# Kernel optimization log

Hardware: AMD Instinct MI355X
Metric: run time of the kernel (lower is better)

## Reference

```python
import jax, jax.numpy as jnp
import numpy as np
import math

N_HEAD = 16
N_EMBD = 1024
BLOCK_SIZE = 2048
B, T = 2, 2048
R = 32.0
MAX_SPAN = float(BLOCK_SIZE)
SPAN_REG = 2e-06
PERIOD_MIN, PERIOD_MAX = 2.0, 4.0
RATIO_MIN, RATIO_MAX = -0.25, 0.25


def setup_inputs() -> dict:
    key = jax.random.key(0)
    ks = jax.random.split(key, 5)
    x = jax.random.normal(ks[0], (B, T, N_EMBD), dtype=jnp.float32)
    # scale weights like nn.Linear init to keep logits sane
    w_attn = jax.random.normal(ks[1], (N_EMBD, 3 * N_EMBD), dtype=jnp.float32) * 0.02
    b_attn = jnp.zeros((3 * N_EMBD,), dtype=jnp.float32)
    w_proj = jax.random.normal(ks[2], (N_EMBD, N_EMBD), dtype=jnp.float32) * 0.02
    b_proj = jnp.zeros((N_EMBD,), dtype=jnp.float32)
    span_params = jnp.zeros((N_HEAD,), dtype=jnp.float32)
    # torch init: period uniform in [2,4] -> logit weight space; ratio 0 -> logit(0.5)=0
    init_period = jax.random.uniform(ks[3], (N_HEAD,), dtype=jnp.float32) * (PERIOD_MAX - PERIOD_MIN) + PERIOD_MIN
    pn = (init_period - PERIOD_MIN) / (PERIOD_MAX - PERIOD_MIN)
    period_weight = jnp.log(pn) - jnp.log1p(-pn)  # logit
    ratio_weight = jnp.zeros((N_HEAD,), dtype=jnp.float32)
    return {"x": x, "w_attn": w_attn, "b_attn": b_attn, "w_proj": w_proj,
            "b_proj": b_proj, "span_params": span_params,
            "period_weight": period_weight, "ratio_weight": ratio_weight}


def _forward(x, w_attn, b_attn, w_proj, b_proj, span_params, period_weight, ratio_weight):
    Bb, Tt, C = x.shape
    D = C // N_HEAD
    qkv = x @ w_attn + b_attn  # [B,T,3C]
    q, k, v = jnp.split(qkv, 3, axis=-1)
    q = q.reshape(Bb, Tt, N_HEAD, D)
    k = k.reshape(Bb, Tt, N_HEAD, D)
    v = v.reshape(Bb, Tt, N_HEAD, D)
    scale = 1.0 / math.sqrt(D)
    att = jnp.einsum('bihd,bjhd->bhij', q, k) * scale  # [B,H,T,T]

    pos = jnp.arange(Tt, dtype=jnp.float32)
    rel = pos[:, None] - pos[None, :]          # [T,T]
    causal = rel >= 0.0
    rel_c = jnp.maximum(rel, 0.0)              # clamp(min=0)

    clamped_spans = jax.nn.sigmoid(span_params) * MAX_SPAN  # [H]
    # span mask: clamp((R - rel + span)/R, 0, 1); non-causal (rel->inf) -> 0
    mask_pos = jnp.where(causal[None, :, :],
                         jnp.clip((R - rel[None, :, :] + clamped_spans[:, None, None]) / R, 0.0, 1.0),
                         0.0)  # [H,T,T]

    period = PERIOD_MIN + (PERIOD_MAX - PERIOD_MIN) * jax.nn.sigmoid(period_weight)  # [H]
    ratio = RATIO_MIN + (RATIO_MAX - RATIO_MIN) * jax.nn.sigmoid(ratio_weight)       # [H]
    amplitude = period / 4.0
    offset = period * ratio
    wave = 0.5 * (jnp.cos(2.0 * math.pi * rel_c[None, :, :] / period[:, None, None]) + 1.0) \
           * amplitude[:, None, None] + 0.5 + offset[:, None, None]
    wave = jnp.clip(wave, 0.0, 1.0)  # [H,T,T]
    loss_terms = 1.0 / period + 2.0 * ratio - 1.0 / PERIOD_MAX - 2.0 * RATIO_MIN  # [H]

    mask = mask_pos * wave  # [H,T,T]

    att = jnp.where(causal[None, None, :, :], att, -jnp.inf)
    att_max = jnp.max(att, axis=-1, keepdims=True)
    att_exp = jnp.exp(att - att_max)
    weighted = att_exp * mask[None]  # [B,H,T,T]
    att = weighted / jnp.sum(weighted, axis=-1, keepdims=True)

    y = jnp.einsum('bhij,bjhd->bihd', att, v).reshape(Bb, Tt, C)
    y = y @ w_proj + b_proj

    span_loss = SPAN_REG * jnp.sum((clamped_spans + R) * loss_terms) / N_HEAD
    return y, span_loss


def reference(x, w_attn, b_attn, w_proj, b_proj, span_params, period_weight, ratio_weight):
    return _forward(x, w_attn, b_attn, w_proj, b_proj, span_params, period_weight, ratio_weight)
```

## Files before the change

kernel.cpp:

```cpp
#include <hip/hip_runtime.h>
#include <math.h>
#include <float.h>

#define NHEAD 16
#define DHEAD 64
#define SEQT  2048
#define NB    2
#define CEMB  1024
#define C3    3072

typedef __attribute__((ext_vector_type(8))) short  s16x8;
typedef __attribute__((ext_vector_type(4))) short  s16x4;
typedef __attribute__((ext_vector_type(8))) unsigned short u16x8;
typedef __attribute__((ext_vector_type(4))) unsigned short u16x4;
typedef __attribute__((ext_vector_type(4))) float  f32x4;

__device__ __forceinline__ float sigmoidf_(float x) { return 1.0f / (1.0f + expf(-x)); }

__device__ __forceinline__ unsigned short f2b(float f) {
    __bf16 b = (__bf16)f;
    return __builtin_bit_cast(unsigned short, b);
}

__device__ __forceinline__ void gload16(const void* g, void* l) {
    __builtin_amdgcn_global_load_lds(
        (const __attribute__((address_space(1))) void*)g,
        (__attribute__((address_space(3))) void*)l, 16, 0, 0);
}

__global__ __launch_bounds__(256) void convert_bf16(const float* __restrict__ s,
                                                    unsigned short* __restrict__ d)
{
    int i = (blockIdx.x * 256 + threadIdx.x) * 4;
    float4 v = *reinterpret_cast<const float4*>(s + i);
    u16x4 o = { f2b(v.x), f2b(v.y), f2b(v.z), f2b(v.w) };
    *reinterpret_cast<u16x4*>(d + i) = o;
}

__global__ __launch_bounds__(256) void transpose_convert(
    const float* __restrict__ src, unsigned short* __restrict__ dst,
    int rows, int cols)
{
    __shared__ float t[64][65];
    const int tid = threadIdx.x;
    const int c0 = blockIdx.x * 64, r0 = blockIdx.y * 64;
    const int tr = tid >> 4, tc = tid & 15;
#pragma unroll
    for (int l = 0; l < 4; ++l) {
        int r = l * 16 + tr;
        float4 vv = *reinterpret_cast<const float4*>(
            &src[(size_t)(r0 + r) * cols + c0 + tc * 4]);
        t[r][tc * 4 + 0] = vv.x; t[r][tc * 4 + 1] = vv.y;
        t[r][tc * 4 + 2] = vv.z; t[r][tc * 4 + 3] = vv.w;
    }
    __syncthreads();
#pragma unroll
    for (int l = 0; l < 4; ++l) {
        int n = l * 16 + tr;
        u16x4 o4 = { f2b(t[tc * 4 + 0][n]), f2b(t[tc * 4 + 1][n]),
                     f2b(t[tc * 4 + 2][n]), f2b(t[tc * 4 + 3][n]) };
        *reinterpret_cast<u16x4*>(&dst[(size_t)(c0 + n) * rows + r0 + tc * 4]) = o4;
    }
}

__global__ void build_ltab(const float* __restrict__ sp, const float* __restrict__ pw,
                           const float* __restrict__ rw, float* __restrict__ ltab)
{
    const int h = blockIdx.x;
    const float span   = sigmoidf_(sp[h]) * 2048.0f;
    const float period = 2.0f + 2.0f * sigmoidf_(pw[h]);
    const float ratio  = -0.25f + 0.5f * sigmoidf_(rw[h]);
    const float amp    = period * 0.25f;
    const float off    = period * ratio;
    for (int rel = threadIdx.x; rel < SEQT; rel += blockDim.x) {
        float mp = fminf(fmaxf((32.0f - (float)rel + span) * 0.03125f, 0.0f), 1.0f);
        float wv = 0.5f * (cosf(6.283185307179586f * (float)rel / period) + 1.0f) * amp
                   + 0.5f + off;
        wv = fminf(fmaxf(wv, 0.0f), 1.0f);
        float m = mp * wv;
        ltab[h * SEQT + rel] = (m > 0.0f) ? (log2f(m) - 8.0f) : -1e30f;
    }
}

template<int N_, int MODE>
__global__ __launch_bounds__(256) void mfma_gemm(
    const unsigned short* __restrict__ A, const unsigned short* __restrict__ Wt,
    const float* __restrict__ bias, float* __restrict__ outf,
    unsigned short* __restrict__ qo, unsigned short* __restrict__ ko,
    unsigned short* __restrict__ vo)
{
    __shared__ unsigned short As[128 * 64];
    __shared__ unsigned short Bs[128 * 64];
    char* AsB = (char*)As;
    char* BsB = (char*)Bs;

    const int tid  = threadIdx.x;
    const int lane = tid & 63;
    const int wid  = tid >> 6;
    const int wm   = wid >> 1, wn = wid & 1;
    const int g    = lane >> 4, l15 = lane & 15;
    const int m0   = blockIdx.y * 128, n0 = blockIdx.x * 128;

    const int srow = lane >> 3;
    const int skel = 8 * ((lane & 7) ^ srow);
    const int swz  = (lane & 7) << 4;

    f32x4 acc[4][4];
#pragma unroll
    for (int i = 0; i < 4; ++i)
#pragma unroll
        for (int j = 0; j < 4; ++j) acc[i][j] = (f32x4){0.f, 0.f, 0.f, 0.f};

    for (int kt = 0; kt < 16; ++kt) {
        const int k0 = kt * 64;
#pragma unroll
        for (int it = 0; it < 4; ++it) {
            int cc = wid * 4 + it;
            int row = cc * 8 + srow;
            gload16(A  + (size_t)(m0 + row) * 1024 + k0 + skel, AsB + cc * 1024);
            gload16(Wt + (size_t)(n0 + row) * 1024 + k0 + skel, BsB + cc * 1024);
        }
        __syncthreads();
#pragma unroll
        for (int kk = 0; kk < 2; ++kk) {
            s16x8 af[4], bfr[4];
#pragma unroll
            for (int mf = 0; mf < 4; ++mf) {
                int m = wm * 64 + mf * 16 + l15;
                af[mf] = *reinterpret_cast<const s16x8*>(
                    AsB + m * 128 + ((kk * 64 + g * 16) ^ swz));
            }
#pragma unroll
            for (int nf = 0; nf < 4; ++nf) {
                int n = wn * 64 + nf * 16 + l15;
                bfr[nf] = *reinterpret_cast<const s16x8*>(
                    BsB + n * 128 + ((kk * 64 + g * 16) ^ swz));
            }
#pragma unroll
            for (int mf = 0; mf < 4; ++mf)
#pragma unroll
                for (int nf = 0; nf < 4; ++nf)
                    acc[mf][nf] = __builtin_amdgcn_mfma_f32_16x16x32_bf16(
                        af[mf], bfr[nf], acc[mf][nf], 0, 0, 0);
        }
        __syncthreads();
    }

#pragma unroll
    for (int mf = 0; mf < 4; ++mf)
#pragma unroll
        for (int nf = 0; nf < 4; ++nf) {
            const int n = n0 + wn * 64 + nf * 16 + l15;
            const int mb = m0 + wm * 64 + mf * 16 + 4 * g;
            const float bs = bias[n];
            if (MODE == 0) {
                const int which = n >> 10;
                const int cc = n & 1023;
                const int hh = cc >> 6, dd = cc & 63;
                const int t0 = mb & (SEQT - 1);
                const int bb = mb >> 11;
                if (which == 2) {
                    u16x4 pk;
#pragma unroll
                    for (int r = 0; r < 4; ++r) pk[r] = f2b(acc[mf][nf][r] + bs);
                    *reinterpret_cast<u16x4*>(
                        &vo[(((size_t)bb * NHEAD + hh) * DHEAD + dd) * SEQT + t0]) = pk;
                } else {
                    unsigned short* dst = (which == 0) ? qo : ko;
#pragma unroll
                    for (int r = 0; r < 4; ++r)
                        dst[(((size_t)bb * NHEAD + hh) * SEQT + t0 + r) * DHEAD + dd] =
                            f2b(acc[mf][nf][r] + bs);
                }
            } else {
#pragma unroll
                for (int r = 0; r < 4; ++r)
                    outf[(size_t)(mb + r) * N_ + n] = acc[mf][nf][r] + bs;
            }
        }
}

__global__ __launch_bounds__(256) void attn_mfma(
    const unsigned short* __restrict__ q, const unsigned short* __restrict__ k,
    const unsigned short* __restrict__ vt, const float* __restrict__ ltab,
    const float* __restrict__ span_p, unsigned short* __restrict__ y)
{
    __shared__ unsigned short Ks[2][64 * 64];
    __shared__ unsigned short Vs[2][64 * 64];

    const int tid  = threadIdx.x;
    const int lane = tid & 63;
    const int w    = tid >> 6;
    const int g    = lane >> 4, l15 = lane & 15;

    const int wgid = blockIdx.x + gridDim.x * blockIdx.y;
    const int xcd  = wgid & 7;
    const int idx  = wgid >> 3;
    const int bh   = (idx >> 5) * 8 + xcd;
    const int qt   = idx & 31;
    const int q0   = qt * 64;
    const int b    = bh >> 4, h = bh & 15;

    const float span = sigmoidf_(span_p[h]) * 2048.0f;
    const float thr  = 32.0f + span;
    const float* lt  = ltab + h * SEQT;

    const size_t base = (size_t)bh * SEQT * DHEAD;
    const unsigned short* qb  = q  + base;
    const unsigned short* kb  = k  + base;
    const unsigned short* vtb = vt + base;

    s16x8 qa[2];
    {
        const char* qrow = (const char*)(qb + (size_t)(q0 + 16 * w + l15) * DHEAD);
        qa[0] = *reinterpret_cast<const s16x8*>(qrow + g * 16);
        qa[1] = *reinterpret_cast<const s16x8*>(qrow + 64 + g * 16);
    }

    f32x4 oa[4];
#pragma unroll
    for (int i = 0; i < 4; ++i) oa[i] = (f32x4){0.f, 0.f, 0.f, 0.f};
    float lrp = 0.f;

    const int srow = lane >> 3;
    const int skel = 8 * ((lane & 7) ^ srow);
    const int swz  = (lane & 7) << 4;
    const int qrel = q0 + 16 * w + l15;
    const float SCL = 0.18033688f;

    int jstart = 0;
    {
        float lim = (float)(q0 - 63) - thr;
        if (lim >= 0.0f) jstart = (((int)lim) >> 6) * 64 + 64;
    }

    auto STAGE = [&](int bsel, int j0s) {
#pragma unroll
        for (int it = 0; it < 2; ++it) {
            int cc = w * 2 + it;
            gload16(kb  + (size_t)(j0s + cc * 8 + srow) * DHEAD + skel,
                    (char*)Ks[bsel] + cc * 1024);
            gload16(vtb + (size_t)(cc * 8 + srow) * SEQT + j0s + skel,
                    (char*)Vs[bsel] + cc * 1024);
        }
    };

    STAGE(0, jstart);
    __syncthreads();
    int cur = 0;

    for (int j0 = jstart; j0 <= q0; j0 += 64) {
        if (j0 + 64 <= q0) STAGE(cur ^ 1, j0 + 64);

        f32x4 st[4];
#pragma unroll
        for (int nf = 0; nf < 4; ++nf) st[nf] = (f32x4){0.f, 0.f, 0.f, 0.f};
#pragma unroll
        for (int kk = 0; kk < 2; ++kk)
#pragma unroll
            for (int nf = 0; nf < 4; ++nf) {
                int c = nf * 16 + l15;
                s16x8 kf = *reinterpret_cast<const s16x8*>(
                    (char*)Ks[cur] + c * 128 + ((kk * 64 + g * 16) ^ swz));
                st[nf] = __builtin_amdgcn_mfma_f32_16x16x32_bf16(kf, qa[kk], st[nf], 0, 0, 0);
            }

        const int r0 = qrel - j0;
        float pvv[4][4];
#pragma unroll
        for (int nf = 0; nf < 4; ++nf)
#pragma unroll
            for (int r = 0; r < 4; ++r) {
                int rel = r0 - 16 * nf - 4 * g - r;
                float p = 0.f;
                if (rel >= 0) p = exp2f(fmaf(st[nf][r], SCL, lt[rel]));
                pvv[nf][r] = p;
                lrp += p;
            }

        s16x8 pa[2];
#pragma unroll
        for (int kk = 0; kk < 2; ++kk)
#pragma unroll
            for (int half = 0; half < 2; ++half)
#pragma unroll
                for (int r = 0; r < 4; ++r)
                    pa[kk][half * 4 + r] = (short)f2b(pvv[kk * 2 + half][r]);

#pragma unroll
        for (int kk = 0; kk < 2; ++kk)
#pragma unroll
            for (int nfd = 0; nfd < 4; ++nfd) {
                const char* vrow = (const char*)Vs[cur] + (nfd * 16 + l15) * 128;
                int o1 = (kk * 64 + g * 8) ^ swz;
                int o2 = (kk * 64 + g * 8 + 32) ^ swz;
                s16x4 lo = *reinterpret_cast<const s16x4*>(vrow + o1);
                s16x4 hi = *reinterpret_cast<const s16x4*>(vrow + o2);
                s16x8 vf;
#pragma unroll
                for (int e = 0; e < 4; ++e) { vf[e] = lo[e]; vf[4 + e] = hi[e]; }
                oa[nfd] = __builtin_amdgcn_mfma_f32_16x16x32_bf16(pa[kk], vf, oa[nfd], 0, 0, 0);
            }

        __syncthreads();
        cur ^= 1;
    }

    float lf = lrp;
    lf += __shfl_xor(lf, 16, 64);
    lf += __shfl_xor(lf, 32, 64);

#pragma unroll
    for (int r = 0; r < 4; ++r) {
        int src = (lane & 48) | (4 * g + r);
        float inv = 1.0f / __shfl(lf, src, 64);
        int gr = q0 + 16 * w + 4 * g + r;
#pragma unroll
        for (int nfd = 0; nfd < 4; ++nfd)
            y[((size_t)b * SEQT + gr) * CEMB + h * 64 + nfd * 16 + l15] =
                f2b(oa[nfd][r] * inv);
    }
}

__global__ void span_loss_kernel(const float* __restrict__ sp,
                                 const float* __restrict__ pw,
                                 const float* __restrict__ rw,
                                 float* __restrict__ out)
{
    int lane = threadIdx.x;
    float val = 0.f;
    if (lane < NHEAD) {
        float span   = sigmoidf_(sp[lane]) * 2048.0f;
        float period = 2.0f + 2.0f * sigmoidf_(pw[lane]);
        float ratio  = -0.25f + 0.5f * sigmoidf_(rw[lane]);
        float ltm = 1.0f / period + 2.0f * ratio - 0.25f + 0.5f;
        val = (span + 32.0f) * ltm;
    }
#pragma unroll
    for (int o = 1; o < 16; o <<= 1) val += __shfl_xor(val, o, 64);
    if (lane == 0) out[0] = 2e-6f * val / 16.0f;
}

extern "C" void kernel_launch(void* const* d_in, const int* in_sizes, int n_in,
                              void* d_out, int out_size, void* d_ws, size_t ws_size,
                              hipStream_t stream)
{
    const float* x        = (const float*)d_in[0];
    const float* w_attn   = (const float*)d_in[1];
    const float* b_attn   = (const float*)d_in[2];
    const float* w_proj   = (const float*)d_in[3];
    const float* b_proj   = (const float*)d_in[4];
    const float* span_p   = (const float*)d_in[5];
    const float* period_w = (const float*)d_in[6];
    const float* ratio_w  = (const float*)d_in[7];

    char* ws = (char*)d_ws;
    unsigned short* xb  = (unsigned short*)(ws);
    unsigned short* wT  = (unsigned short*)(ws + ((size_t)8  << 20));
    unsigned short* wpT = (unsigned short*)(ws + ((size_t)14 << 20));
    unsigned short* qb  = (unsigned short*)(ws + ((size_t)16 << 20));
    unsigned short* kb  = (unsigned short*)(ws + ((size_t)24 << 20));
    unsigned short* vt  = (unsigned short*)(ws + ((size_t)32 << 20));
    float*          lt  = (float*)         (ws + ((size_t)40 << 20));
    unsigned short* y1  = xb;

    float* out = (float*)d_out;
    const size_t PLANE = (size_t)NB * SEQT * CEMB;

    convert_bf16<<<4096, 256, 0, stream>>>(x, xb);
    transpose_convert<<<dim3(C3 / 64, CEMB / 64), 256, 0, stream>>>(w_attn, wT, CEMB, C3);
    transpose_convert<<<dim3(CEMB / 64, CEMB / 64), 256, 0, stream>>>(w_proj, wpT, CEMB, CEMB);
    build_ltab<<<NHEAD, 256, 0, stream>>>(span_p, period_w, ratio_w, lt);

    mfma_gemm<C3, 0><<<dim3(C3 / 128, (NB * SEQT) / 128), 256, 0, stream>>>(
        xb, wT, b_attn, nullptr, qb, kb, vt);

    attn_mfma<<<dim3(SEQT / 64, NB * NHEAD), 256, 0, stream>>>(
        qb, kb, vt, lt, span_p, y1);

    mfma_gemm<CEMB, 1><<<dim3(CEMB / 128, (NB * SEQT) / 128), 256, 0, stream>>>(
        y1, wpT, b_proj, out, nullptr, nullptr, nullptr);

    span_loss_kernel<<<1, 64, 0, stream>>>(span_p, period_w, ratio_w, out + PLANE);
}
```

Before: 229.7 us.

## Use 32x32 MFMA with 128-row query tiles and balanced causal tile ordering

Result: slower. 253.8 us (+10.5%).

```diff
diff --git a/kernel.cpp b/kernel.cpp
--- a/kernel.cpp
+++ b/kernel.cpp
@@ -9,11 +9,11 @@
 #define CEMB  1024
 #define C3    3072
 
-typedef __attribute__((ext_vector_type(8))) short  s16x8;
-typedef __attribute__((ext_vector_type(4))) short  s16x4;
-typedef __attribute__((ext_vector_type(8))) unsigned short u16x8;
-typedef __attribute__((ext_vector_type(4))) unsigned short u16x4;
-typedef __attribute__((ext_vector_type(4))) float  f32x4;
+typedef __attribute__((ext_vector_type(8)))  short s16x8;
+typedef __attribute__((ext_vector_type(4)))  short s16x4;
+typedef __attribute__((ext_vector_type(4)))  unsigned short u16x4;
+typedef __attribute__((ext_vector_type(4)))  float f32x4;
+typedef __attribute__((ext_vector_type(16))) float f32x16;
 
 __device__ __forceinline__ float sigmoidf_(float x) { return 1.0f / (1.0f + expf(-x)); }
 
@@ -191,14 +191,16 @@
     const int tid  = threadIdx.x;
     const int lane = tid & 63;
     const int w    = tid >> 6;
-    const int g    = lane >> 4, l15 = lane & 15;
+    const int q31  = lane & 31, hi = lane >> 5;
 
     const int wgid = blockIdx.x + gridDim.x * blockIdx.y;
     const int xcd  = wgid & 7;
-    const int idx  = wgid >> 3;
-    const int bh   = (idx >> 5) * 8 + xcd;
-    const int qt   = idx & 31;
-    const int q0   = qt * 64;
+    const int li   = wgid >> 3;
+    const int bhl  = li >> 4;
+    const int i2   = ((li & 15) + 4 * bhl) & 15;
+    const int qt   = (i2 & 1) ? (15 - (i2 >> 1)) : (i2 >> 1);
+    const int bh   = bhl * 8 + xcd;
+    const int q0   = qt * 128;
     const int b    = bh >> 4, h = bh & 15;
 
     const float span = sigmoidf_(span_p[h]) * 2048.0f;
@@ -206,33 +208,32 @@
     const float* lt  = ltab + h * SEQT;
 
     const size_t base = (size_t)bh * SEQT * DHEAD;
-    const unsigned short* qb  = q  + base;
     const unsigned short* kb  = k  + base;
     const unsigned short* vtb = vt + base;
 
-    s16x8 qa[2];
+    const int qbase = q0 + 32 * w;
+
+    s16x8 qa[4];
     {
-        const char* qrow = (const char*)(qb + (size_t)(q0 + 16 * w + l15) * DHEAD);
-        qa[0] = *reinterpret_cast<const s16x8*>(qrow + g * 16);
-        qa[1] = *reinterpret_cast<const s16x8*>(qrow + 64 + g * 16);
-    }
-
-    f32x4 oa[4];
-#pragma unroll
-    for (int i = 0; i < 4; ++i) oa[i] = (f32x4){0.f, 0.f, 0.f, 0.f};
+        const char* qrow = (const char*)(q + base + (size_t)(qbase + q31) * DHEAD);
+#pragma unroll
+        for (int c = 0; c < 4; ++c)
+            qa[c] = *reinterpret_cast<const s16x8*>(qrow + c * 32 + hi * 16);
+    }
+
+    f32x16 oa0, oa1;
+#pragma unroll
+    for (int i = 0; i < 16; ++i) { oa0[i] = 0.f; oa1[i] = 0.f; }
     float lrp = 0.f;
 
     const int srow = lane >> 3;
     const int skel = 8 * ((lane & 7) ^ srow);
     const int swz  = (lane & 7) << 4;
-    const int qrel = q0 + 16 * w + l15;
     const float SCL = 0.18033688f;
 
     int jstart = 0;
-    {
-        float lim = (float)(q0 - 63) - thr;
-        if (lim >= 0.0f) jstart = (((int)lim) >> 6) * 64 + 64;
-    }
+    {   float lim = (float)(q0 - 63) - thr;
+        if (lim >= 0.0f) jstart = (((int)lim) >> 6) * 64 + 64; }
 
     auto STAGE = [&](int bsel, int j0s) {
 #pragma unroll
@@ -249,76 +250,87 @@
     __syncthreads();
     int cur = 0;
 
-    for (int j0 = jstart; j0 <= q0; j0 += 64) {
-        if (j0 + 64 <= q0) STAGE(cur ^ 1, j0 + 64);
-
-        f32x4 st[4];
-#pragma unroll
-        for (int nf = 0; nf < 4; ++nf) st[nf] = (f32x4){0.f, 0.f, 0.f, 0.f};
-#pragma unroll
-        for (int kk = 0; kk < 2; ++kk)
-#pragma unroll
-            for (int nf = 0; nf < 4; ++nf) {
-                int c = nf * 16 + l15;
-                s16x8 kf = *reinterpret_cast<const s16x8*>(
-                    (char*)Ks[cur] + c * 128 + ((kk * 64 + g * 16) ^ swz));
-                st[nf] = __builtin_amdgcn_mfma_f32_16x16x32_bf16(kf, qa[kk], st[nf], 0, 0, 0);
-            }
-
-        const int r0 = qrel - j0;
-        float pvv[4][4];
-#pragma unroll
-        for (int nf = 0; nf < 4; ++nf)
-#pragma unroll
-            for (int r = 0; r < 4; ++r) {
-                int rel = r0 - 16 * nf - 4 * g - r;
-                float p = 0.f;
-                if (rel >= 0) p = exp2f(fmaf(st[nf][r], SCL, lt[rel]));
-                pvv[nf][r] = p;
-                lrp += p;
-            }
-
-        s16x8 pa[2];
-#pragma unroll
-        for (int kk = 0; kk < 2; ++kk)
-#pragma unroll
-            for (int half = 0; half < 2; ++half)
-#pragma unroll
-                for (int r = 0; r < 4; ++r)
-                    pa[kk][half * 4 + r] = (short)f2b(pvv[kk * 2 + half][r]);
-
-#pragma unroll
-        for (int kk = 0; kk < 2; ++kk)
-#pragma unroll
-            for (int nfd = 0; nfd < 4; ++nfd) {
-                const char* vrow = (const char*)Vs[cur] + (nfd * 16 + l15) * 128;
-                int o1 = (kk * 64 + g * 8) ^ swz;
-                int o2 = (kk * 64 + g * 8 + 32) ^ swz;
-                s16x4 lo = *reinterpret_cast<const s16x4*>(vrow + o1);
-                s16x4 hi = *reinterpret_cast<const s16x4*>(vrow + o2);
-                s16x8 vf;
-#pragma unroll
-                for (int e = 0; e < 4; ++e) { vf[e] = lo[e]; vf[4 + e] = hi[e]; }
-                oa[nfd] = __builtin_amdgcn_mfma_f32_16x16x32_bf16(pa[kk], vf, oa[nfd], 0, 0, 0);
-            }
+    const int jend = q0 + 64;
+    for (int j0 = jstart; j0 <= jend; j0 += 64) {
+        if (j0 < jend) STAGE(cur ^ 1, j0 + 64);
+
+        const bool active = (j0 <= qbase + 31) &&
+                            ((float)(qbase - j0 - 63) < thr);
+        if (active) {
+            f32x16 st0, st1;
+#pragma unroll
+            for (int i = 0; i < 16; ++i) { st0[i] = 0.f; st1[i] = 0.f; }
+#pragma unroll
+            for (int c = 0; c < 4; ++c) {
+                const int dof = (c * 32 + hi * 16) ^ swz;
+                s16x8 kf0 = *reinterpret_cast<const s16x8*>(
+                    (const char*)Ks[cur] + q31 * 128 + dof);
+                s16x8 kf1 = *reinterpret_cast<const s16x8*>(
+                    (const char*)Ks[cur] + (32 + q31) * 128 + dof);
+                st0 = __builtin_amdgcn_mfma_f32_32x32x16_bf16(kf0, qa[c], st0, 0, 0, 0);
+                st1 = __builtin_amdgcn_mfma_f32_32x32x16_bf16(kf1, qa[c], st1, 0, 0, 0);
+            }
+
+            const int relq = qbase + q31 - j0 - 4 * hi;
+            float p0[16], p1[16];
+            float lacc = 0.f;
+#pragma unroll
+            for (int r = 0; r < 16; ++r) {
+                int koff = (r & 3) + 8 * (r >> 2);
+                int rel0 = relq - koff;
+                int rel1 = rel0 - 32;
+                float a0 = 0.f, a1 = 0.f;
+                if (rel0 >= 0) a0 = exp2f(fmaf(st0[r], SCL, lt[rel0]));
+                if (rel1 >= 0) a1 = exp2f(fmaf(st1[r], SCL, lt[rel1]));
+                p0[r] = a0; p1[r] = a1;
+                lacc += a0 + a1;
+            }
+            lrp += lacc;
+
+            s16x8 pa00, pa01, pa10, pa11;
+#pragma unroll
+            for (int e = 0; e < 8; ++e) {
+                pa00[e] = (short)f2b(p0[e]);
+                pa01[e] = (short)f2b(p0[8 + e]);
+                pa10[e] = (short)f2b(p1[e]);
+                pa11[e] = (short)f2b(p1[8 + e]);
+            }
+
+#pragma unroll
+            for (int td = 0; td < 2; ++td) {
+                const char* vrow = (const char*)Vs[cur] + (32 * td + q31) * 128;
+                f32x16 oo = td ? oa1 : oa0;
+#pragma unroll
+                for (int t = 0; t < 2; ++t)
+#pragma unroll
+                    for (int n = 0; n < 2; ++n) {
+                        int bse = 64 * t + 32 * n + 8 * hi;
+                        s16x4 lo4 = *reinterpret_cast<const s16x4*>(vrow + (bse ^ swz));
+                        s16x4 hi4 = *reinterpret_cast<const s16x4*>(vrow + ((bse | 16) ^ swz));
+                        s16x8 vf;
+#pragma unroll
+                        for (int e = 0; e < 4; ++e) { vf[e] = lo4[e]; vf[4 + e] = hi4[e]; }
+                        s16x8 paf = t ? (n ? pa11 : pa10) : (n ? pa01 : pa00);
+                        oo = __builtin_amdgcn_mfma_f32_32x32x16_bf16(paf, vf, oo, 0, 0, 0);
+                    }
+                if (td) oa1 = oo; else oa0 = oo;
+            }
+        }
 
         __syncthreads();
         cur ^= 1;
     }
 
-    float lf = lrp;
-    lf += __shfl_xor(lf, 16, 64);
-    lf += __shfl_xor(lf, 32, 64);
-
-#pragma unroll
-    for (int r = 0; r < 4; ++r) {
-        int src = (lane & 48) | (4 * g + r);
-        float inv = 1.0f / __shfl(lf, src, 64);
-        int gr = q0 + 16 * w + 4 * g + r;
-#pragma unroll
-        for (int nfd = 0; nfd < 4; ++nfd)
-            y[((size_t)b * SEQT + gr) * CEMB + h * 64 + nfd * 16 + l15] =
-                f2b(oa[nfd][r] * inv);
+    float lf = lrp + __shfl_xor(lrp, 32, 64);
+
+    unsigned short* yb = y + (size_t)b * SEQT * CEMB + h * 64;
+#pragma unroll
+    for (int r = 0; r < 16; ++r) {
+        int qrow = (r & 3) + 8 * (r >> 2) + 4 * hi;
+        float inv = 1.0f / __shfl(lf, qrow, 64);
+        size_t rowoff = (size_t)(qbase + qrow) * CEMB;
+        yb[rowoff + q31]      = f2b(oa0[r] * inv);
+        yb[rowoff + 32 + q31] = f2b(oa1[r] * inv);
     }
 }
 
@@ -375,7 +387,7 @@
     mfma_gemm<C3, 0><<<dim3(C3 / 128, (NB * SEQT) / 128), 256, 0, stream>>>(
         xb, wT, b_attn, nullptr, qb, kb, vt);
 
-    attn_mfma<<<dim3(SEQT / 64, NB * NHEAD), 256, 0, stream>>>(
+    attn_mfma<<<dim3(SEQT / 128, NB * NHEAD), 256, 0, stream>>>(
         qb, kb, vt, lt, span_p, y1);
 
     mfma_gemm<CEMB, 1><<<dim3(CEMB / 128, (NB * SEQT) / 128), 256, 0, stream>>>(
```
